# Optimization experiments

Measured on AMD Instinct MI355X. Metric: run time of the kernel, lower is better.

Reference implementation:

```python
import jax, jax.numpy as jnp
import numpy as np

N = 10000   # nodes
K = 8       # out-degree per node (uniform)
E = N * K   # edges
D = 64      # d_embed (also per-head dim: projection is d_embed -> d_embed*n_heads)
H = 8       # n_heads
DE = 16     # d_e_embed (also per-edge-head dim)
EH = 4      # e_heads
EPS = 1e-16


def seg_softmax(src, index, num):
    # torch_geometric.utils.softmax: per-segment max-subtract, exp, normalize
    mx = jax.ops.segment_max(src, index, num_segments=num)
    mx = jnp.where(jnp.isfinite(mx), mx, 0.0)
    ex = jnp.exp(src - mx[index])
    s = jax.ops.segment_sum(ex, index, num_segments=num)
    return ex / (s[index] + EPS)


def _lin(k, out_d, in_d):
    # xavier-uniform-ish weight, zero bias (matches init_weights)
    bound = float(np.sqrt(6.0 / (in_d + out_d)))
    W = jax.random.uniform(k, (out_d, in_d), jnp.float32, -bound, bound)
    return W, jnp.zeros((out_d,), jnp.float32)


def setup_inputs() -> dict:
    key = jax.random.key(0)
    ks = jax.random.split(key, 12)
    x = jax.random.normal(ks[0], (N, D), jnp.float32)
    row0 = jnp.repeat(jnp.arange(N, dtype=jnp.int32), K)          # sorted sources
    row1 = jax.random.randint(ks[1], (E,), 0, N, jnp.int32)        # random targets
    edge_index = jnp.stack([row0, row1])                           # [2, E]
    # n^3 pair indices (uniform degree => closed form matching torch helper)
    eiq = jnp.repeat(jnp.arange(E, dtype=jnp.int32), K)            # repeat_interleave within node block
    eik = jnp.broadcast_to(jnp.arange(E, dtype=jnp.int32).reshape(N, 1, K), (N, K, K)).reshape(-1)  # tile within block
    edge_features = jax.random.normal(ks[2], (E, DE), jnp.float32)
    Wq, bq = _lin(ks[3], D * H, D)
    Wk, bk = _lin(ks[4], D * H, D)
    Wv, bv = _lin(ks[5], D * H, D)
    Wlin, blin = _lin(ks[6], D, H * D)
    Weq, beq = _lin(ks[7], DE * EH, DE)
    Wev, bev = _lin(ks[8], DE * EH, DE)
    Wek, bek = _lin(ks[9], DE * EH, H)
    Wel, bel = _lin(ks[10], H, EH * DE)
    Wele, bele = _lin(ks[11], DE, H)
    return dict(x=x, edge_features=edge_features,
                Wq=Wq, bq=bq, Wk=Wk, bk=bk, Wv=Wv, bv=bv, Wlin=Wlin, blin=blin,
                Weq=Weq, beq=beq, Wev=Wev, bev=bev, Wek=Wek, bek=bek,
                Wel=Wel, bel=bel, Wele=Wele, bele=bele,
                edge_index=edge_index, eiq=eiq, eik=eik)


def reference(x, edge_features, Wq, bq, Wk, bk, Wv, bv, Wlin, blin,
              Weq, beq, Wev, bev, Wek, bek, Wel, bel, Wele, bele,
              edge_index, eiq, eik):
    e0, e1 = edge_index[0], edge_index[1]
    nq = (x @ Wq.T + bq).reshape(N, H, D)
    nk = (x @ Wk.T + bk).reshape(N, H, D)
    nv = (x @ Wv.T + bv).reshape(N, H, D)
    # per-edge scaled dot product: [E, H]
    sqk = (nq[e0] * nk[e1]).sum(-1) / jnp.sqrt(jnp.float32(D))
    # --- edge attention over edge-edge pairs ---
    eq = (edge_features @ Weq.T + beq).reshape(E, EH, DE)
    ev = (edge_features @ Wev.T + bev).reshape(E, EH, DE)
    ek = (sqk @ Wek.T + bek).reshape(E, EH, DE)
    seqk = (eq[eiq] * ek[eik]).sum(-1) / jnp.sqrt(jnp.float32(DE))   # [P, EH]
    att_e = seg_softmax(seqk, eiq, E)
    eout = jax.ops.segment_sum(att_e[:, :, None] * ev[eik], eiq, num_segments=E)  # [E, EH, DE]
    edge_emb = eout.reshape(E, EH * DE) @ Wel.T + bel                # [E, H]
    # --- node attention with edge-modulated scores ---
    att_n = seg_softmax(edge_emb + sqk, e0, N)                       # [E, H]
    node = jax.ops.segment_sum(att_n[:, :, None] * nv[e1], e0, num_segments=N)    # [N, H, D]
    node_embeddings = node.reshape(N, H * D) @ Wlin.T + blin         # [N, D]
    edge_embeddings = edge_emb @ Wele.T + bele                       # [E, DE]
    return node_embeddings, edge_embeddings
```

## Files before the change

### kernel.cpp

```cpp
#include <hip/hip_runtime.h>

typedef unsigned short u16;
typedef unsigned int   u32;

#define N_NODES 10000
#define N_EDGES 80000

typedef __attribute__((ext_vector_type(8))) short bf16x8;
typedef __attribute__((ext_vector_type(4))) float fx4;
#define MFMA16(a, b, c) __builtin_amdgcn_mfma_f32_16x16x32_bf16(a, b, c, 0, 0, 0)

__device__ __forceinline__ u16 f2bf(float f) {
    union { float f; u32 i; } c; c.f = f;
    u32 u = c.i;
    u32 r = (u + 0x7fffu + ((u >> 16) & 1u)) >> 16;
    return (u16)r;
}
__device__ __forceinline__ float bf2f(u16 u) {
    union { u32 i; float f; } c; c.i = ((u32)u) << 16; return c.f;
}
__device__ __forceinline__ void unpack8(uint4 w, float* v) {
    union { u32 i; float f; } c;
    c.i = w.x << 16; v[0] = c.f; c.i = w.x & 0xffff0000u; v[1] = c.f;
    c.i = w.y << 16; v[2] = c.f; c.i = w.y & 0xffff0000u; v[3] = c.f;
    c.i = w.z << 16; v[4] = c.f; c.i = w.z & 0xffff0000u; v[5] = c.f;
    c.i = w.w << 16; v[6] = c.f; c.i = w.w & 0xffff0000u; v[7] = c.f;
}

__device__ __forceinline__ void wsync() {
    asm volatile("s_waitcnt lgkmcnt(0)" ::: "memory");
    __builtin_amdgcn_wave_barrier();
}


__device__ __forceinline__ void stage_w(const float* src, int rstride,
                                        u16* wh, u16* wl, int t) {
    const int row = t >> 2, seg = t & 3;
    const float* p = src + (long)row * rstride + seg * 16;
    float v[16];
    #pragma unroll
    for (int q = 0; q < 4; ++q) *(float4*)&v[q * 4] = *(const float4*)(p + q * 4);
    u16 hh[16], ll[16];
    #pragma unroll
    for (int j = 0; j < 16; ++j) {
        u16 hi = f2bf(v[j]);
        hh[j] = hi;
        ll[j] = f2bf(v[j] - bf2f(hi));
    }
    const int base = row * 72 + seg * 16;
    *(uint4*)&wh[base]     = *(uint4*)&hh[0];
    *(uint4*)&wh[base + 8] = *(uint4*)&hh[8];
    *(uint4*)&wl[base]     = *(uint4*)&ll[0];
    *(uint4*)&wl[base + 8] = *(uint4*)&ll[8];
}

__device__ __forceinline__ void load_a64(const float* m, int arow, int ko,
                                         bf16x8 ah[2], bf16x8 al[2]) {
    if (arow < N_NODES) {
        #pragma unroll
        for (int ks = 0; ks < 2; ++ks) {
            const float* p = m + (long)arow * 64 + ks * 32 + ko;
            float v[8];
            *(float4*)&v[0] = *(const float4*)p;
            *(float4*)&v[4] = *(const float4*)(p + 4);
            #pragma unroll
            for (int j = 0; j < 8; ++j) {
                u16 hi = f2bf(v[j]);
                ah[ks][j] = (short)hi;
                al[ks][j] = (short)f2bf(v[j] - bf2f(hi));
            }
        }
    } else {
        #pragma unroll
        for (int ks = 0; ks < 2; ++ks) { ah[ks] = (bf16x8)0; al[ks] = (bf16x8)0; }
    }
}

__device__ __forceinline__ fx4 gemm3(const bf16x8 ah[2], const bf16x8 al[2],
                                     const u16* wh, const u16* wl,
                                     int colrow, int ko) {
    fx4 acc = {0.f, 0.f, 0.f, 0.f};
    #pragma unroll
    for (int ks = 0; ks < 2; ++ks) {
        const bf16x8 bh = *(const bf16x8*)&wh[colrow * 72 + ks * 32 + ko];
        const bf16x8 bl = *(const bf16x8*)&wl[colrow * 72 + ks * 32 + ko];
        acc = MFMA16(al[ks], bh, acc);
        acc = MFMA16(ah[ks], bl, acc);
        acc = MFMA16(ah[ks], bh, acc);
    }
    return acc;
}

__global__ __launch_bounds__(256) void proj_kernel(
    const float* __restrict__ x,
    const float* __restrict__ Wq, const float* __restrict__ bq,
    const float* __restrict__ Wk, const float* __restrict__ bk,
    const float* __restrict__ Wv, const float* __restrict__ bv,
    const float* __restrict__ Wlin,
    float* __restrict__ NQ, u16* __restrict__ NK, u16* __restrict__ G)
{
    __shared__ __align__(16) u16 wh[64 * 72];
    __shared__ __align__(16) u16 wl[64 * 72];
    __shared__ __align__(16) u16 nvh[4 * 16 * 72];
    __shared__ __align__(16) u16 nvl[4 * 16 * 72];

    const int t  = threadIdx.x;
    const int l  = t & 63, w = t >> 6;
    const int ko = (l >> 4) * 8;
    const int r0 = blockIdx.x * 64;
    const int h  = blockIdx.y;
    const int c0 = h * 64;

    bf16x8 ah[2], al[2];
    load_a64(x, r0 + w * 16 + (l & 15), ko, ah, al);

    fx4 acc[4];

    stage_w(Wq + (long)c0 * 64, 64, wh, wl, t);
    __syncthreads();
    #pragma unroll
    for (int cf = 0; cf < 4; ++cf)
        acc[cf] = gemm3(ah, al, wh, wl, cf * 16 + (l & 15), ko);
    #pragma unroll
    for (int cf = 0; cf < 4; ++cf) {
        const int col = c0 + cf * 16 + (l & 15);
        const float bias = bq[col];
        #pragma unroll
        for (int j = 0; j < 4; ++j) {
            const int gr = r0 + w * 16 + (l >> 4) * 4 + j;
            if (gr < N_NODES) NQ[(long)gr * 512 + col] = acc[cf][j] + bias;
        }
    }
    __syncthreads();

    stage_w(Wk + (long)c0 * 64, 64, wh, wl, t);
    __syncthreads();
    #pragma unroll
    for (int cf = 0; cf < 4; ++cf)
        acc[cf] = gemm3(ah, al, wh, wl, cf * 16 + (l & 15), ko);
    #pragma unroll
    for (int cf = 0; cf < 4; ++cf) {
        const int col = c0 + cf * 16 + (l & 15);
        const float bias = bk[col];
        #pragma unroll
        for (int j = 0; j < 4; ++j) {
            const int gr = r0 + w * 16 + (l >> 4) * 4 + j;
            if (gr < N_NODES) NK[(long)gr * 512 + col] = f2bf(acc[cf][j] + bias);
        }
    }
    __syncthreads();

    stage_w(Wv + (long)c0 * 64, 64, wh, wl, t);
    __syncthreads();
    #pragma unroll
    for (int cf = 0; cf < 4; ++cf)
        acc[cf] = gemm3(ah, al, wh, wl, cf * 16 + (l & 15), ko);
    #pragma unroll
    for (int cf = 0; cf < 4; ++cf) {
        const int col = cf * 16 + (l & 15);
        const float bias = bv[c0 + col];
        #pragma unroll
        for (int j = 0; j < 4; ++j) {
            const int rloc = (l >> 4) * 4 + j;
            float v = acc[cf][j] + bias;
            u16 hi = f2bf(v);
            nvh[w * 1152 + rloc * 72 + col] = hi;
            nvl[w * 1152 + rloc * 72 + col] = f2bf(v - bf2f(hi));
        }
    }
    __syncthreads();
    stage_w(Wlin + c0, 512, wh, wl, t);
    __syncthreads();

    bf16x8 a2h[2], a2l[2];
    #pragma unroll
    for (int ks = 0; ks < 2; ++ks) {
        a2h[ks] = *(const bf16x8*)&nvh[w * 1152 + (l & 15) * 72 + ks * 32 + ko];
        a2l[ks] = *(const bf16x8*)&nvl[w * 1152 + (l & 15) * 72 + ks * 32 + ko];
    }
    #pragma unroll
    for (int cf = 0; cf < 4; ++cf)
        acc[cf] = gemm3(a2h, a2l, wh, wl, cf * 16 + (l & 15), ko);

    #pragma unroll
    for (int cf = 0; cf < 4; ++cf) {
        const int col = c0 + cf * 16 + (l & 15);
        #pragma unroll
        for (int j = 0; j < 4; ++j) {
            const int gr = r0 + w * 16 + (l >> 4) * 4 + j;
            if (gr < N_NODES) G[(long)gr * 512 + col] = f2bf(acc[cf][j]);
        }
    }
}

#define SLAB_F 2272
__global__ __launch_bounds__(256) void node_kernel(
    const float* __restrict__ ef, const int* __restrict__ e1,
    const float* __restrict__ NQ, const u16* __restrict__ NK,
    const u16* __restrict__ G,
    const float* __restrict__ Weq, const float* __restrict__ beq,
    const float* __restrict__ Wev, const float* __restrict__ bev,
    const float* __restrict__ Wek, const float* __restrict__ bek,
    const float* __restrict__ Wel, const float* __restrict__ bel,
    const float* __restrict__ Wele, const float* __restrict__ bele,
    const float* __restrict__ blin,
    float* __restrict__ out_node, float* __restrict__ out_edge)
{
    __shared__ __align__(16) float well[8 * 68];
    __shared__ __align__(16) float slabs[4][SLAB_F];

    const int t   = threadIdx.x;
    const int t64 = t & 63;
    const int wv  = t >> 6;
    const int n   = (int)__builtin_amdgcn_readfirstlane(blockIdx.x * 4 + wv);

    float* S      = slabs[wv];
    float* eqb    = S;
    float* ekb    = S + 544;
    float* eob    = eqb;
    float* sl     = S + 1088;
    float* efl    = S + 1376;
    u16*   gbuf   = (u16*)S;
    float* sqk_l  = S + 2080;
    float* emb_l  = S + 2144;
    float* attn_l = S + 2208;

    int tg[8];
    #pragma unroll
    for (int i = 0; i < 8; ++i) tg[i] = e1[n * 8 + i];

    float q8[8];
    {
        const float4* p = (const float4*)(NQ + (long)n * 512 + t64 * 8);
        *(float4*)&q8[0] = p[0];
        *(float4*)&q8[4] = p[1];
    }
    uint4 kreg[8];
    #pragma unroll
    for (int i = 0; i < 8; ++i)
        kreg[i] = *(const uint4*)(NK + (long)tg[i] * 512 + t64 * 8);

    float2 efv = ((const float2*)(ef + (long)n * 128))[t64];

    float wq16[16], wv16[16], wk8[8], wele8[8];
    {
        const float4* p = (const float4*)(Weq + t64 * 16);
        #pragma unroll
        for (int q4 = 0; q4 < 4; ++q4) *(float4*)&wq16[q4 * 4] = p[q4];
        const float4* q = (const float4*)(Wev + t64 * 16);
        #pragma unroll
        for (int q4 = 0; q4 < 4; ++q4) *(float4*)&wv16[q4 * 4] = q[q4];
        const float4* r = (const float4*)(Wek + t64 * 8);
        *(float4*)&wk8[0] = r[0]; *(float4*)&wk8[4] = r[1];
        const float4* s = (const float4*)(Wele + (t64 & 15) * 8);
        *(float4*)&wele8[0] = s[0]; *(float4*)&wele8[4] = s[1];
    }
    const float beqv = beq[t64], bevv = bev[t64], bekv = bek[t64];
    const float bele_t = bele[t64 & 15];
    const float blin_t = blin[t64];

    #pragma unroll
    for (int rep = 0; rep < 2; ++rep) {
        const int idx = rep * 256 + t;
        well[(idx >> 6) * 68 + (idx & 63)] = Wel[idx];
    }
    efl[2 * t64] = efv.x; efl[2 * t64 + 1] = efv.y;

    {
        float part[8];
        #pragma unroll
        for (int i = 0; i < 8; ++i) {
            float kv[8]; unpack8(kreg[i], kv);
            float s = q8[0] * kv[0] + q8[1] * kv[1] + q8[2] * kv[2] + q8[3] * kv[3]
                    + q8[4] * kv[4] + q8[5] * kv[5] + q8[6] * kv[6] + q8[7] * kv[7];
            part[i] = s;
        }
        #pragma unroll
        for (int m = 1; m <= 4; m <<= 1) {
            #pragma unroll
            for (int i = 0; i < 8; ++i) part[i] += __shfl_xor(part[i], m);
        }
        const int h8 = t64 >> 3, dc = t64 & 7;
        sqk_l[dc * 8 + h8] = part[dc] * 0.125f;
    }
    __syncthreads();

    float ev_reg[8];
    #pragma unroll
    for (int i = 0; i < 8; ++i) {
        float aq = beqv, av = bevv;
        #pragma unroll
        for (int q = 0; q < 4; ++q) {
            float4 f = *(const float4*)&efl[i * 16 + q * 4];
            aq += f.x * wq16[q * 4] + f.y * wq16[q * 4 + 1] + f.z * wq16[q * 4 + 2] + f.w * wq16[q * 4 + 3];
            av += f.x * wv16[q * 4] + f.y * wv16[q * 4 + 1] + f.z * wv16[q * 4 + 2] + f.w * wv16[q * 4 + 3];
        }
        float ak = bekv;
        #pragma unroll
        for (int q = 0; q < 2; ++q) {
            float4 s = *(const float4*)&sqk_l[i * 8 + q * 4];
            ak += s.x * wk8[q * 4] + s.y * wk8[q * 4 + 1] + s.z * wk8[q * 4 + 2] + s.w * wk8[q * 4 + 3];
        }
        eqb[i * 68 + t64] = aq; ekb[i * 68 + t64] = ak;
        ev_reg[i] = av;
    }
    wsync();

    {
        const int i = t64 >> 3, j = t64 & 7;
        #pragma unroll
        for (int eh = 0; eh < 4; ++eh) {
            float acc = 0.f;
            #pragma unroll
            for (int q = 0; q < 4; ++q) {
                float4 a = *(const float4*)&eqb[i * 68 + eh * 16 + q * 4];
                float4 b = *(const float4*)&ekb[j * 68 + eh * 16 + q * 4];
                acc += a.x * b.x + a.y * b.y + a.z * b.z + a.w * b.w;
            }
            sl[eh * 72 + i * 8 + j] = acc * 0.25f;
        }
    }
    wsync();

    if (t64 < 32) {
        const int i = t64 >> 2, eh = t64 & 3;
        float4 v0 = *(const float4*)&sl[eh * 72 + i * 8];
        float4 v1 = *(const float4*)&sl[eh * 72 + i * 8 + 4];
        float mx = fmaxf(fmaxf(fmaxf(v0.x, v0.y), fmaxf(v0.z, v0.w)),
                         fmaxf(fmaxf(v1.x, v1.y), fmaxf(v1.z, v1.w)));
        float e0 = __expf(v0.x - mx), e1_ = __expf(v0.y - mx);
        float e2 = __expf(v0.z - mx), e3  = __expf(v0.w - mx);
        float e4 = __expf(v1.x - mx), e5  = __expf(v1.y - mx);
        float e6 = __expf(v1.z - mx), e7  = __expf(v1.w - mx);
        float inv = 1.f / (e0 + e1_ + e2 + e3 + e4 + e5 + e6 + e7 + 1e-16f);
        float4 w0 = {e0 * inv, e1_ * inv, e2 * inv, e3 * inv};
        float4 w1 = {e4 * inv, e5 * inv, e6 * inv, e7 * inv};
        *(float4*)&sl[eh * 72 + i * 8]     = w0;
        *(float4*)&sl[eh * 72 + i * 8 + 4] = w1;
    }
    wsync();

    {
        const int eh = t64 >> 4;
        #pragma unroll
        for (int i = 0; i < 8; ++i) {
            float4 s0 = *(const float4*)&sl[eh * 72 + i * 8];
            float4 s1 = *(const float4*)&sl[eh * 72 + i * 8 + 4];
            float acc = s0.x * ev_reg[0] + s0.y * ev_reg[1]
                      + s0.z * ev_reg[2] + s0.w * ev_reg[3]
                      + s1.x * ev_reg[4] + s1.y * ev_reg[5]
                      + s1.z * ev_reg[6] + s1.w * ev_reg[7];
            eob[i * 68 + t64] = acc;
        }
    }
    wsync();

    uint4 greg[8];
    {
        const int i = t64 >> 3, c8 = t64 & 7;
        const uint4* gp = (const uint4*)(G + (long)tg[i] * 512);
        #pragma unroll
        for (int q = 0; q < 8; ++q) greg[q] = gp[c8 + q * 8];
    }

    {
        const int i = t64 >> 3, h = t64 & 7;
        float acc = bel[h];
        #pragma unroll
        for (int q = 0; q < 16; ++q) {
            float4 a  = *(const float4*)&eob[i * 68 + q * 4];
            float4 ww = *(const float4*)&well[h * 68 + q * 4];
            acc += a.x * ww.x + a.y * ww.y + a.z * ww.z + a.w * ww.w;
        }
        emb_l[i * 8 + h] = acc;
    }
    wsync();

    #pragma unroll
    for (int rep = 0; rep < 2; ++rep) {
        const int idx = rep * 64 + t64;
        const int i = idx >> 4;
        float acc = bele_t;
        #pragma unroll
        for (int h = 0; h < 8; ++h) acc += emb_l[i * 8 + h] * wele8[h];
        out_edge[(long)n * 128 + idx] = acc;
    }

    if (t64 < 8) {
        const int h = t64;
        float lg[8], mx = -1e30f;
        #pragma unroll
        for (int i = 0; i < 8; ++i) { lg[i] = emb_l[i * 8 + h] + sqk_l[i * 8 + h]; mx = fmaxf(mx, lg[i]); }
        float sum = 0.f;
        #pragma unroll
        for (int i = 0; i < 8; ++i) { float e = __expf(lg[i] - mx); attn_l[i * 8 + h] = e; sum += e; }
        float inv = 1.f / (sum + 1e-16f);
        #pragma unroll
        for (int i = 0; i < 8; ++i) attn_l[i * 8 + h] *= inv;
    }

    {
        const int i = t64 >> 3, c8 = t64 & 7;
        #pragma unroll
        for (int q = 0; q < 8; ++q)
            *(uint4*)&gbuf[i * 520 + (c8 + q * 8) * 8] = greg[q];
    }
    wsync();

    {
        float acc = blin_t;
        #pragma unroll
        for (int i = 0; i < 8; ++i) {
            float4 a0 = *(const float4*)&attn_l[i * 8];
            float4 a1 = *(const float4*)&attn_l[i * 8 + 4];
            const u16* gr = &gbuf[i * 520];
            acc += a0.x * bf2f(gr[0 * 64 + t64]) + a0.y * bf2f(gr[1 * 64 + t64])
                 + a0.z * bf2f(gr[2 * 64 + t64]) + a0.w * bf2f(gr[3 * 64 + t64])
                 + a1.x * bf2f(gr[4 * 64 + t64]) + a1.y * bf2f(gr[5 * 64 + t64])
                 + a1.z * bf2f(gr[6 * 64 + t64]) + a1.w * bf2f(gr[7 * 64 + t64]);
        }
        out_node[(long)n * 64 + t64] = acc;
    }
}

extern "C" void kernel_launch(void* const* d_in, const int* in_sizes, int n_in,
                              void* d_out, int out_size, void* d_ws, size_t ws_size,
                              hipStream_t stream) {
    (void)in_sizes; (void)n_in; (void)out_size; (void)ws_size;
    const float* x    = (const float*)d_in[0];
    const float* ef   = (const float*)d_in[1];
    const float* Wq   = (const float*)d_in[2];
    const float* bq   = (const float*)d_in[3];
    const float* Wk   = (const float*)d_in[4];
    const float* bk   = (const float*)d_in[5];
    const float* Wv   = (const float*)d_in[6];
    const float* bv   = (const float*)d_in[7];
    const float* Wlin = (const float*)d_in[8];
    const float* blin = (const float*)d_in[9];
    const float* Weq  = (const float*)d_in[10];
    const float* beq  = (const float*)d_in[11];
    const float* Wev  = (const float*)d_in[12];
    const float* bev  = (const float*)d_in[13];
    const float* Wek  = (const float*)d_in[14];
    const float* bek  = (const float*)d_in[15];
    const float* Wel  = (const float*)d_in[16];
    const float* bel  = (const float*)d_in[17];
    const float* Wele = (const float*)d_in[18];
    const float* bele = (const float*)d_in[19];
    const int* edge_index = (const int*)d_in[20];
    const int* e1 = edge_index + N_EDGES;

    float* out_node = (float*)d_out;
    float* out_edge = (float*)d_out + 640000;

    char* ws = (char*)d_ws;
    u16*   NK = (u16*)ws;
    u16*   G  = (u16*)(ws + 10240000);
    float* NQ = (float*)(ws + 20480000);

    proj_kernel<<<dim3(157, 8), 256, 0, stream>>>(x, Wq, bq, Wk, bk, Wv, bv, Wlin,
                                                  NQ, NK, G);
    node_kernel<<<2500, 256, 0, stream>>>(ef, e1, NQ, NK, G,
                                          Weq, beq, Wev, bev, Wek, bek,
                                          Wel, bel, Wele, bele, blin,
                                          out_node, out_edge);
}
```

Before: 174.5 us.

## Process two nodes per wave and prefetch second node's gathers during first

Each wavefront now handles two consecutive nodes instead of one, halving the grid. The weight and bias register loads and the shared Wel staging are amortized across both nodes. The Q/K/edge-feature gathers for the second node are issued before the first node's final output phase, so their latency overlaps that work. In exchange there are fewer blocks in flight (1250 on a large GPU), more live registers, and the second node's work runs serially within the wave.

Measured after the change: 184.5 us. 5.8% more time.

```diff
diff --git a/kernel.cpp b/kernel.cpp
--- a/kernel.cpp
+++ b/kernel.cpp
@@ -212,7 +212,8 @@
     const int t   = threadIdx.x;
     const int t64 = t & 63;
     const int wv  = t >> 6;
-    const int n   = (int)__builtin_amdgcn_readfirstlane(blockIdx.x * 4 + wv);
+    const int nA  = (int)__builtin_amdgcn_readfirstlane(blockIdx.x * 8 + wv * 2);
+    const int nB  = nA + 1;
 
     float* S      = slabs[wv];
     float* eqb    = S;
@@ -225,22 +226,22 @@
     float* emb_l  = S + 2144;
     float* attn_l = S + 2208;
 
-    int tg[8];
-    #pragma unroll
-    for (int i = 0; i < 8; ++i) tg[i] = e1[n * 8 + i];
+    int tgA[8], tgB[8];
+    #pragma unroll
+    for (int i = 0; i < 8; ++i) { tgA[i] = e1[nA * 8 + i]; tgB[i] = e1[nB * 8 + i]; }
 
     float q8[8];
     {
-        const float4* p = (const float4*)(NQ + (long)n * 512 + t64 * 8);
+        const float4* p = (const float4*)(NQ + (long)nA * 512 + t64 * 8);
         *(float4*)&q8[0] = p[0];
         *(float4*)&q8[4] = p[1];
     }
     uint4 kreg[8];
     #pragma unroll
     for (int i = 0; i < 8; ++i)
-        kreg[i] = *(const uint4*)(NK + (long)tg[i] * 512 + t64 * 8);
-
-    float2 efv = ((const float2*)(ef + (long)n * 128))[t64];
+        kreg[i] = *(const uint4*)(NK + (long)tgA[i] * 512 + t64 * 8);
+
+    float2 efv = ((const float2*)(ef + (long)nA * 128))[t64];
 
     float wq16[16], wv16[16], wk8[8], wele8[8];
     {
@@ -266,14 +267,13 @@
     }
     efl[2 * t64] = efv.x; efl[2 * t64 + 1] = efv.y;
 
-    {
+    auto sq_butterfly = [&]() {
         float part[8];
         #pragma unroll
         for (int i = 0; i < 8; ++i) {
             float kv[8]; unpack8(kreg[i], kv);
-            float s = q8[0] * kv[0] + q8[1] * kv[1] + q8[2] * kv[2] + q8[3] * kv[3]
+            part[i] = q8[0] * kv[0] + q8[1] * kv[1] + q8[2] * kv[2] + q8[3] * kv[3]
                     + q8[4] * kv[4] + q8[5] * kv[5] + q8[6] * kv[6] + q8[7] * kv[7];
-            part[i] = s;
         }
         #pragma unroll
         for (int m = 1; m <= 4; m <<= 1) {
@@ -282,132 +282,132 @@
         }
         const int h8 = t64 >> 3, dc = t64 & 7;
         sqk_l[dc * 8 + h8] = part[dc] * 0.125f;
-    }
-    __syncthreads();
-
-    float ev_reg[8];
-    #pragma unroll
-    for (int i = 0; i < 8; ++i) {
-        float aq = beqv, av = bevv;
-        #pragma unroll
-        for (int q = 0; q < 4; ++q) {
-            float4 f = *(const float4*)&efl[i * 16 + q * 4];
-            aq += f.x * wq16[q * 4] + f.y * wq16[q * 4 + 1] + f.z * wq16[q * 4 + 2] + f.w * wq16[q * 4 + 3];
-            av += f.x * wv16[q * 4] + f.y * wv16[q * 4 + 1] + f.z * wv16[q * 4 + 2] + f.w * wv16[q * 4 + 3];
-        }
-        float ak = bekv;
-        #pragma unroll
-        for (int q = 0; q < 2; ++q) {
-            float4 s = *(const float4*)&sqk_l[i * 8 + q * 4];
-            ak += s.x * wk8[q * 4] + s.y * wk8[q * 4 + 1] + s.z * wk8[q * 4 + 2] + s.w * wk8[q * 4 + 3];
-        }
-        eqb[i * 68 + t64] = aq; ekb[i * 68 + t64] = ak;
-        ev_reg[i] = av;
-    }
-    wsync();
-
-    {
-        const int i = t64 >> 3, j = t64 & 7;
-        #pragma unroll
-        for (int eh = 0; eh < 4; ++eh) {
-            float acc = 0.f;
+    };
+
+    auto phases2to8 = [&](int n, const int* tg) {
+        float ev_reg[8];
+        #pragma unroll
+        for (int i = 0; i < 8; ++i) {
+            float aq = beqv, av = bevv;
             #pragma unroll
             for (int q = 0; q < 4; ++q) {
-                float4 a = *(const float4*)&eqb[i * 68 + eh * 16 + q * 4];
-                float4 b = *(const float4*)&ekb[j * 68 + eh * 16 + q * 4];
-                acc += a.x * b.x + a.y * b.y + a.z * b.z + a.w * b.w;
-            }
-            sl[eh * 72 + i * 8 + j] = acc * 0.25f;
-        }
-    }
-    wsync();
-
-    if (t64 < 32) {
-        const int i = t64 >> 2, eh = t64 & 3;
-        float4 v0 = *(const float4*)&sl[eh * 72 + i * 8];
-        float4 v1 = *(const float4*)&sl[eh * 72 + i * 8 + 4];
-        float mx = fmaxf(fmaxf(fmaxf(v0.x, v0.y), fmaxf(v0.z, v0.w)),
-                         fmaxf(fmaxf(v1.x, v1.y), fmaxf(v1.z, v1.w)));
-        float e0 = __expf(v0.x - mx), e1_ = __expf(v0.y - mx);
-        float e2 = __expf(v0.z - mx), e3  = __expf(v0.w - mx);
-        float e4 = __expf(v1.x - mx), e5  = __expf(v1.y - mx);
-        float e6 = __expf(v1.z - mx), e7  = __expf(v1.w - mx);
-        float inv = 1.f / (e0 + e1_ + e2 + e3 + e4 + e5 + e6 + e7 + 1e-16f);
-        float4 w0 = {e0 * inv, e1_ * inv, e2 * inv, e3 * inv};
-        float4 w1 = {e4 * inv, e5 * inv, e6 * inv, e7 * inv};
-        *(float4*)&sl[eh * 72 + i * 8]     = w0;
-        *(float4*)&sl[eh * 72 + i * 8 + 4] = w1;
-    }
-    wsync();
-
-    {
-        const int eh = t64 >> 4;
-        #pragma unroll
-        for (int i = 0; i < 8; ++i) {
-            float4 s0 = *(const float4*)&sl[eh * 72 + i * 8];
-            float4 s1 = *(const float4*)&sl[eh * 72 + i * 8 + 4];
-            float acc = s0.x * ev_reg[0] + s0.y * ev_reg[1]
-                      + s0.z * ev_reg[2] + s0.w * ev_reg[3]
-                      + s1.x * ev_reg[4] + s1.y * ev_reg[5]
-                      + s1.z * ev_reg[6] + s1.w * ev_reg[7];
-            eob[i * 68 + t64] = acc;
-        }
-    }
-    wsync();
-
-    uint4 greg[8];
-    {
-        const int i = t64 >> 3, c8 = t64 & 7;
-        const uint4* gp = (const uint4*)(G + (long)tg[i] * 512);
-        #pragma unroll
-        for (int q = 0; q < 8; ++q) greg[q] = gp[c8 + q * 8];
-    }
-
-    {
-        const int i = t64 >> 3, h = t64 & 7;
-        float acc = bel[h];
-        #pragma unroll
-        for (int q = 0; q < 16; ++q) {
-            float4 a  = *(const float4*)&eob[i * 68 + q * 4];
-            float4 ww = *(const float4*)&well[h * 68 + q * 4];
-            acc += a.x * ww.x + a.y * ww.y + a.z * ww.z + a.w * ww.w;
-        }
-        emb_l[i * 8 + h] = acc;
-    }
-    wsync();
-
-    #pragma unroll
-    for (int rep = 0; rep < 2; ++rep) {
-        const int idx = rep * 64 + t64;
-        const int i = idx >> 4;
-        float acc = bele_t;
-        #pragma unroll
-        for (int h = 0; h < 8; ++h) acc += emb_l[i * 8 + h] * wele8[h];
-        out_edge[(long)n * 128 + idx] = acc;
-    }
-
-    if (t64 < 8) {
-        const int h = t64;
-        float lg[8], mx = -1e30f;
-        #pragma unroll
-        for (int i = 0; i < 8; ++i) { lg[i] = emb_l[i * 8 + h] + sqk_l[i * 8 + h]; mx = fmaxf(mx, lg[i]); }
-        float sum = 0.f;
-        #pragma unroll
-        for (int i = 0; i < 8; ++i) { float e = __expf(lg[i] - mx); attn_l[i * 8 + h] = e; sum += e; }
-        float inv = 1.f / (sum + 1e-16f);
-        #pragma unroll
-        for (int i = 0; i < 8; ++i) attn_l[i * 8 + h] *= inv;
-    }
-
-    {
-        const int i = t64 >> 3, c8 = t64 & 7;
-        #pragma unroll
-        for (int q = 0; q < 8; ++q)
-            *(uint4*)&gbuf[i * 520 + (c8 + q * 8) * 8] = greg[q];
-    }
-    wsync();
-
-    {
+                float4 f = *(const float4*)&efl[i * 16 + q * 4];
+                aq += f.x * wq16[q * 4] + f.y * wq16[q * 4 + 1] + f.z * wq16[q * 4 + 2] + f.w * wq16[q * 4 + 3];
+                av += f.x * wv16[q * 4] + f.y * wv16[q * 4 + 1] + f.z * wv16[q * 4 + 2] + f.w * wv16[q * 4 + 3];
+            }
+            float ak = bekv;
+            #pragma unroll
+            for (int q = 0; q < 2; ++q) {
+                float4 s = *(const float4*)&sqk_l[i * 8 + q * 4];
+                ak += s.x * wk8[q * 4] + s.y * wk8[q * 4 + 1] + s.z * wk8[q * 4 + 2] + s.w * wk8[q * 4 + 3];
+            }
+            eqb[i * 68 + t64] = aq; ekb[i * 68 + t64] = ak;
+            ev_reg[i] = av;
+        }
+        wsync();
+
+        {
+            const int i = t64 >> 3, j = t64 & 7;
+            #pragma unroll
+            for (int eh = 0; eh < 4; ++eh) {
+                float acc = 0.f;
+                #pragma unroll
+                for (int q = 0; q < 4; ++q) {
+                    float4 a = *(const float4*)&eqb[i * 68 + eh * 16 + q * 4];
+                    float4 b = *(const float4*)&ekb[j * 68 + eh * 16 + q * 4];
+                    acc += a.x * b.x + a.y * b.y + a.z * b.z + a.w * b.w;
+                }
+                sl[eh * 72 + i * 8 + j] = acc * 0.25f;
+            }
+        }
+        wsync();
+
+        if (t64 < 32) {
+            const int i = t64 >> 2, eh = t64 & 3;
+            float4 v0 = *(const float4*)&sl[eh * 72 + i * 8];
+            float4 v1 = *(const float4*)&sl[eh * 72 + i * 8 + 4];
+            float mx = fmaxf(fmaxf(fmaxf(v0.x, v0.y), fmaxf(v0.z, v0.w)),
+                             fmaxf(fmaxf(v1.x, v1.y), fmaxf(v1.z, v1.w)));
+            float e0 = __expf(v0.x - mx), e1_ = __expf(v0.y - mx);
+            float e2 = __expf(v0.z - mx), e3  = __expf(v0.w - mx);
+            float e4 = __expf(v1.x - mx), e5  = __expf(v1.y - mx);
+            float e6 = __expf(v1.z - mx), e7  = __expf(v1.w - mx);
+            float inv = 1.f / (e0 + e1_ + e2 + e3 + e4 + e5 + e6 + e7 + 1e-16f);
+            float4 w0 = {e0 * inv, e1_ * inv, e2 * inv, e3 * inv};
+            float4 w1 = {e4 * inv, e5 * inv, e6 * inv, e7 * inv};
+            *(float4*)&sl[eh * 72 + i * 8]     = w0;
+            *(float4*)&sl[eh * 72 + i * 8 + 4] = w1;
+        }
+        wsync();
+
+        {
+            const int eh = t64 >> 4;
+            #pragma unroll
+            for (int i = 0; i < 8; ++i) {
+                float4 s0 = *(const float4*)&sl[eh * 72 + i * 8];
+                float4 s1 = *(const float4*)&sl[eh * 72 + i * 8 + 4];
+                float acc = s0.x * ev_reg[0] + s0.y * ev_reg[1]
+                          + s0.z * ev_reg[2] + s0.w * ev_reg[3]
+                          + s1.x * ev_reg[4] + s1.y * ev_reg[5]
+                          + s1.z * ev_reg[6] + s1.w * ev_reg[7];
+                eob[i * 68 + t64] = acc;
+            }
+        }
+        wsync();
+
+        uint4 greg[8];
+        {
+            const int i = t64 >> 3, c8 = t64 & 7;
+            const uint4* gp = (const uint4*)(G + (long)tg[i] * 512);
+            #pragma unroll
+            for (int q = 0; q < 8; ++q) greg[q] = gp[c8 + q * 8];
+        }
+
+        {
+            const int i = t64 >> 3, h = t64 & 7;
+            float acc = bel[h];
+            #pragma unroll
+            for (int q = 0; q < 16; ++q) {
+                float4 a  = *(const float4*)&eob[i * 68 + q * 4];
+                float4 ww = *(const float4*)&well[h * 68 + q * 4];
+                acc += a.x * ww.x + a.y * ww.y + a.z * ww.z + a.w * ww.w;
+            }
+            emb_l[i * 8 + h] = acc;
+        }
+        wsync();
+
+        #pragma unroll
+        for (int rep = 0; rep < 2; ++rep) {
+            const int idx = rep * 64 + t64;
+            const int i = idx >> 4;
+            float acc = bele_t;
+            #pragma unroll
+            for (int h = 0; h < 8; ++h) acc += emb_l[i * 8 + h] * wele8[h];
+            out_edge[(long)n * 128 + idx] = acc;
+        }
+
+        if (t64 < 8) {
+            const int h = t64;
+            float lg[8], mx = -1e30f;
+            #pragma unroll
+            for (int i = 0; i < 8; ++i) { lg[i] = emb_l[i * 8 + h] + sqk_l[i * 8 + h]; mx = fmaxf(mx, lg[i]); }
+            float sum = 0.f;
+            #pragma unroll
+            for (int i = 0; i < 8; ++i) { float e = __expf(lg[i] - mx); attn_l[i * 8 + h] = e; sum += e; }
+            float inv = 1.f / (sum + 1e-16f);
+            #pragma unroll
+            for (int i = 0; i < 8; ++i) attn_l[i * 8 + h] *= inv;
+        }
+        {
+            const int i = t64 >> 3, c8 = t64 & 7;
+            #pragma unroll
+            for (int q = 0; q < 8; ++q)
+                *(uint4*)&gbuf[i * 520 + (c8 + q * 8) * 8] = greg[q];
+        }
+        wsync();
+    };
+
+    auto phase9 = [&](int n) {
         float acc = blin_t;
         #pragma unroll
         for (int i = 0; i < 8; ++i) {
@@ -420,7 +420,32 @@
                  + a1.z * bf2f(gr[6 * 64 + t64]) + a1.w * bf2f(gr[7 * 64 + t64]);
         }
         out_node[(long)n * 64 + t64] = acc;
-    }
+    };
+
+    sq_butterfly();
+    __syncthreads();
+
+    phases2to8(nA, tgA);
+
+    {
+        const float4* p = (const float4*)(NQ + (long)nB * 512 + t64 * 8);
+        *(float4*)&q8[0] = p[0];
+        *(float4*)&q8[4] = p[1];
+        #pragma unroll
+        for (int i = 0; i < 8; ++i)
+            kreg[i] = *(const uint4*)(NK + (long)tgB[i] * 512 + t64 * 8);
+        efv = ((const float2*)(ef + (long)nB * 128))[t64];
+    }
+
+    phase9(nA);
+
+    wsync();
+    efl[2 * t64] = efv.x; efl[2 * t64 + 1] = efv.y;
+    sq_butterfly();
+    wsync();
+
+    phases2to8(nB, tgB);
+    phase9(nB);
 }
 
 extern "C" void kernel_launch(void* const* d_in, const int* in_sizes, int n_in,
@@ -460,7 +485,7 @@
 
     proj_kernel<<<dim3(157, 8), 256, 0, stream>>>(x, Wq, bq, Wk, bk, Wv, bv, Wlin,
                                                   NQ, NK, G);
-    node_kernel<<<2500, 256, 0, stream>>>(ef, e1, NQ, NK, G,
+    node_kernel<<<1250, 256, 0, stream>>>(ef, e1, NQ, NK, G,
                                           Weq, beq, Wev, bev, Wek, bek,
                                           Wel, bel, Wele, bele, blin,
                                           out_node, out_edge);
```
